# Performance work log

Measured on AMD Instinct MI355X. Metric: run time of the kernel, lower is better.

## Reference

```python
import jax, jax.numpy as jnp
import numpy as np

B, T, D = 32, 4096, 64
K = 512
COMMITMENT_COST = 0.25


def setup_inputs() -> dict:
    key = jax.random.key(0)
    kz, kw = jax.random.split(key)
    z = jax.random.normal(kz, (B, T, D), dtype=jnp.float32)
    # matches nn.init.uniform_(weight, -1/K, 1/K)
    W = jax.random.uniform(kw, (K, D), dtype=jnp.float32, minval=-1.0 / K, maxval=1.0 / K)
    return {"z": z, "W": W}


def reference(z, W):
    b, t, d = z.shape
    z_flat = z.reshape(-1, d)                                   # [N, D]
    # squared euclidean distances via ||z||^2 + ||w||^2 - 2 z.w
    dist = (jnp.sum(z_flat * z_flat, axis=1, keepdims=True)
            + jnp.sum(W * W, axis=1)
            - 2.0 * z_flat @ W.T)                               # [N, K]
    indices = jnp.argmin(dist, axis=1)                          # [N]
    z_q = W[indices].reshape(b, t, d)                           # gather
    # straight-through estimator
    z_q_st = z + jax.lax.stop_gradient(z_q - z)
    loss = COMMITMENT_COST * jnp.mean((z - jax.lax.stop_gradient(z_q_st)) ** 2)
    return z_q_st, indices.reshape(b, t), loss
```

## Files before the change

### kernel.cpp

```cpp
#include <hip/hip_runtime.h>
#include <hip/hip_bf16.h>
#include <math.h>

#define NROWS 131072
#define KC    512
#define DD    64
#define NELEM (NROWS * DD)

#define OUT_IDX_OFF  NELEM
#define OUT_LOSS_OFF (NELEM + NROWS)

#define MARGIN 3e-5f

#define WSO_CNT   0
#define WSO_LOSS  8
#define WSO_WNORM 64
#define WSO_BH    4096
#define WSO_BL    (WSO_BH + 65536)
#define WSO_LIST  (WSO_BL + 65536)

typedef __attribute__((ext_vector_type(8))) short short8;
typedef __attribute__((ext_vector_type(4))) float f32x4;

__device__ __forceinline__ short f2bf_bits(float f) {
  __hip_bfloat16 h = __float2bfloat16(f);
  short s; __builtin_memcpy(&s, &h, 2); return s;
}
__device__ __forceinline__ float bfbits2f(short s) {
  __hip_bfloat16 h; __builtin_memcpy(&h, &s, 2);
  return __bfloat162float(h);
}
__device__ __forceinline__ void cvt8(const float* __restrict__ p, short8& hi, short8& lo) {
#pragma unroll
  for (int j = 0; j < 8; j++) {
    float f = p[j];
    short hb = f2bf_bits(f);
    float r = f - bfbits2f(hb);
    hi[j] = hb;
    lo[j] = f2bf_bits(r);
  }
}

__device__ __forceinline__ float np_sumsq64(const float* __restrict__ p) {
#pragma clang fp contract(off)
  float r0 = p[0] * p[0], r1 = p[1] * p[1], r2 = p[2] * p[2], r3 = p[3] * p[3];
  float r4 = p[4] * p[4], r5 = p[5] * p[5], r6 = p[6] * p[6], r7 = p[7] * p[7];
  for (int i = 8; i < 64; i += 8) {
    r0 = r0 + p[i + 0] * p[i + 0];
    r1 = r1 + p[i + 1] * p[i + 1];
    r2 = r2 + p[i + 2] * p[i + 2];
    r3 = r3 + p[i + 3] * p[i + 3];
    r4 = r4 + p[i + 4] * p[i + 4];
    r5 = r5 + p[i + 5] * p[i + 5];
    r6 = r6 + p[i + 6] * p[i + 6];
    r7 = r7 + p[i + 7] * p[i + 7];
  }
  return ((r0 + r1) + (r2 + r3)) + ((r4 + r5) + (r6 + r7));
}

__global__ void k_prep(const float* __restrict__ W, short8* __restrict__ Bh,
                       short8* __restrict__ Bl, float* __restrict__ wnorm) {
  int gtid = blockIdx.x * blockDim.x + threadIdx.x;
  int t = gtid >> 7, rem = gtid & 127;
  int h = rem >> 6, L = rem & 63;
  int cw = (t << 4) + (L & 15);
  int dbase = (h << 5) + ((L >> 4) << 3);
  short8 hi, lo;
  cvt8(W + (cw << 6) + dbase, hi, lo);
  Bh[gtid] = hi;
  Bl[gtid] = lo;
  if (gtid < KC) wnorm[gtid] = np_sumsq64(W + (gtid << 6));
}

__global__ __launch_bounds__(256) void k_screen(
    const float* __restrict__ z, const float* __restrict__ W,
    const short8* __restrict__ Bh, const short8* __restrict__ Bl,
    const float* __restrict__ wnorm, float* __restrict__ out,
    int* __restrict__ flagList, int* __restrict__ flagCnt,
    float* __restrict__ lossSum) {
  const int lane = threadIdx.x & 63;
  const int wave = threadIdx.x >> 6;
  const int rowBase = blockIdx.x * 256 + wave * 64;
  const int m = lane & 15, quad = lane >> 4;

  short8 Ah[4][2], Al[4][2];
#pragma unroll
  for (int mt = 0; mt < 4; mt++) {
    const float* zp = z + (size_t)(rowBase + (mt << 4) + m) * DD + (quad << 3);
#pragma unroll
    for (int h = 0; h < 2; h++) cvt8(zp + (h << 5), Ah[mt][h], Al[mt][h]);
  }

  float b1[4][4], b2[4][4];
  int bi[4][4];
#pragma unroll
  for (int mt = 0; mt < 4; mt++)
#pragma unroll
    for (int r = 0; r < 4; r++) { b1[mt][r] = 1e30f; b2[mt][r] = 1e30f; bi[mt][r] = 0; }

  for (int t = 0; t < 32; t++) {
    short8 Bhf[2], Blf[2];
#pragma unroll
    for (int h = 0; h < 2; h++) {
      Bhf[h] = Bh[((t * 2 + h) << 6) + lane];
      Blf[h] = Bl[((t * 2 + h) << 6) + lane];
    }
    float wn = wnorm[(t << 4) + m];

    f32x4 acc[4] = {{0.f, 0.f, 0.f, 0.f}, {0.f, 0.f, 0.f, 0.f},
                    {0.f, 0.f, 0.f, 0.f}, {0.f, 0.f, 0.f, 0.f}};
#pragma unroll
    for (int h = 0; h < 2; h++) {
#pragma unroll
      for (int mt = 0; mt < 4; mt++)
        acc[mt] = __builtin_amdgcn_mfma_f32_16x16x32_bf16(Ah[mt][h], Bhf[h], acc[mt], 0, 0, 0);
#pragma unroll
      for (int mt = 0; mt < 4; mt++)
        acc[mt] = __builtin_amdgcn_mfma_f32_16x16x32_bf16(Al[mt][h], Bhf[h], acc[mt], 0, 0, 0);
#pragma unroll
      for (int mt = 0; mt < 4; mt++)
        acc[mt] = __builtin_amdgcn_mfma_f32_16x16x32_bf16(Ah[mt][h], Blf[h], acc[mt], 0, 0, 0);
    }

    int colv = (t << 4) + m;
#pragma unroll
    for (int mt = 0; mt < 4; mt++)
#pragma unroll
      for (int r = 0; r < 4; r++) {
        float s = fmaf(-2.0f, acc[mt][r], wn);
        if (s < b1[mt][r]) { b2[mt][r] = b1[mt][r]; b1[mt][r] = s; bi[mt][r] = colv; }
        else b2[mt][r] = fminf(b2[mt][r], s);
      }
  }

#pragma unroll
  for (int off = 1; off < 16; off <<= 1) {
#pragma unroll
    for (int mt = 0; mt < 4; mt++)
#pragma unroll
      for (int r = 0; r < 4; r++) {
        float o1 = __shfl_xor(b1[mt][r], off, 64);
        float o2 = __shfl_xor(b2[mt][r], off, 64);
        int oi = __shfl_xor(bi[mt][r], off, 64);
        if (o1 < b1[mt][r] || (o1 == b1[mt][r] && oi < bi[mt][r])) {
          b2[mt][r] = fminf(b1[mt][r], o2);
          b1[mt][r] = o1; bi[mt][r] = oi;
        } else {
          b2[mt][r] = fminf(b2[mt][r], o1);
        }
      }
  }

  float lossAcc = 0.f;
#pragma unroll
  for (int mt = 0; mt < 4; mt++)
#pragma unroll
    for (int lr = 0; lr < 16; lr++) {
      const int q = lr >> 2, r = lr & 3;
      int ki = __shfl(bi[mt][r], q << 4, 64);
      float b1r = __shfl(b1[mt][r], q << 4, 64);
      float b2r = __shfl(b2[mt][r], q << 4, 64);
      int row = rowBase + (mt << 4) + lr;
      float zv = z[(size_t)row * DD + lane];
      float w = W[(ki << 6) + lane];
      float tt = w - zv;
      float o = zv + tt;
      out[(size_t)row * DD + lane] = o;
      float dl = zv - o;
      lossAcc = fmaf(dl, dl, lossAcc);
      if (lane == 0) {
        out[OUT_IDX_OFF + row] = (float)ki;
        if (b2r - b1r < MARGIN) {
          int slot = atomicAdd(flagCnt, 1);
          flagList[slot] = row;
        }
      }
    }

#pragma unroll
  for (int off = 1; off < 64; off <<= 1) lossAcc += __shfl_xor(lossAcc, off, 64);
  if (lane == 0) atomicAdd(lossSum, lossAcc);
}

__global__ void k_refine(const float* __restrict__ z, const float* __restrict__ W,
                         const float* __restrict__ wnp, float* __restrict__ out,
                         const int* __restrict__ flagList,
                         const int* __restrict__ flagCnt,
                         float* __restrict__ lossSum) {
  int nflag = *flagCnt;
  int lane = threadIdx.x & 63;
  int wave = (blockIdx.x * blockDim.x + threadIdx.x) >> 6;
  int nWaves = (gridDim.x * blockDim.x) >> 6;

  for (int f = wave; f < nflag; f += nWaves) {
    int row = flagList[f];
    const float* zr = z + (size_t)row * DD;
    float A = np_sumsq64(zr);

    float best = 1e30f;
    int bk = 0x7fffffff;
#pragma unroll
    for (int j = 0; j < KC / 64; j++) {
      int k = lane + (j << 6);
      const float* wk = W + (k << 6);
      double cd = 0.0;
      for (int d = 0; d < DD; d++) cd = fma((double)zr[d], (double)wk[d], cd);
      float twoC = (float)(2.0 * cd);
      float dist;
      {
#pragma clang fp contract(off)
        float t1 = A + wnp[k];
        dist = t1 - twoC;
      }
      if (dist < best || (dist == best && k < bk)) { best = dist; bk = k; }
    }
#pragma unroll
    for (int off = 1; off < 64; off <<= 1) {
      float ov = __shfl_xor(best, off, 64);
      int ok = __shfl_xor(bk, off, 64);
      if (ov < best || (ov == best && ok < bk)) { best = ov; bk = ok; }
    }

    int kold = (int)out[OUT_IDX_OFF + row];
    if (bk != kold) {
      float zv = zr[lane];
      float wN = W[(bk << 6) + lane];
      float oOld = out[(size_t)row * DD + lane];
      float tN = wN - zv;
      float oN = zv + tN;
      out[(size_t)row * DD + lane] = oN;
      float dN = zv - oN, dO = zv - oOld;
      float delta = dN * dN - dO * dO;
#pragma unroll
      for (int off = 1; off < 64; off <<= 1) delta += __shfl_xor(delta, off, 64);
      if (lane == 0) {
        atomicAdd(lossSum, delta);
        out[OUT_IDX_OFF + row] = (float)bk;
      }
    }
  }
}

__global__ void k_finalize(const float* __restrict__ lossSum, float* __restrict__ out) {
  out[OUT_LOSS_OFF] = 0.25f * (*lossSum) / (float)NELEM;
}

extern "C" void kernel_launch(void* const* d_in, const int* in_sizes, int n_in,
                              void* d_out, int out_size, void* d_ws, size_t ws_size,
                              hipStream_t stream) {
  const float* z = (const float*)d_in[0];
  const float* W = (const float*)d_in[1];
  float* out = (float*)d_out;
  char* ws = (char*)d_ws;

  int* flagCnt = (int*)(ws + WSO_CNT);
  float* lossSum = (float*)(ws + WSO_LOSS);
  float* wnorm = (float*)(ws + WSO_WNORM);
  short8* Bh = (short8*)(ws + WSO_BH);
  short8* Bl = (short8*)(ws + WSO_BL);
  int* flagList = (int*)(ws + WSO_LIST);

  hipMemsetAsync(d_ws, 0, 64, stream);

  k_prep<<<16, 256, 0, stream>>>(W, Bh, Bl, wnorm);
  k_screen<<<NROWS / 256, 256, 0, stream>>>(z, W, Bh, Bl, wnorm, out,
                                            flagList, flagCnt, lossSum);
  k_refine<<<256, 256, 0, stream>>>(z, W, wnorm, out, flagList, flagCnt, lossSum);
  k_finalize<<<1, 1, 0, stream>>>(lossSum, out);
}
```

Before: 189.2 us.

## Fuse codebook prep into screen kernel and finalize loss in refine

```diff
diff --git a/kernel.cpp b/kernel.cpp
--- a/kernel.cpp
+++ b/kernel.cpp
@@ -14,30 +14,29 @@
 
 #define WSO_CNT   0
 #define WSO_LOSS  8
+#define WSO_DONE  16
 #define WSO_WNORM 64
-#define WSO_BH    4096
-#define WSO_BL    (WSO_BH + 65536)
-#define WSO_LIST  (WSO_BL + 65536)
+#define WSO_LIST  4096
 
 typedef __attribute__((ext_vector_type(8))) short short8;
 typedef __attribute__((ext_vector_type(4))) float f32x4;
 
-__device__ __forceinline__ short f2bf_bits(float f) {
+static __device__ __forceinline__ short f2bf(float f) {
   __hip_bfloat16 h = __float2bfloat16(f);
   short s; __builtin_memcpy(&s, &h, 2); return s;
 }
-__device__ __forceinline__ float bfbits2f(short s) {
-  __hip_bfloat16 h; __builtin_memcpy(&h, &s, 2);
-  return __bfloat162float(h);
-}
-__device__ __forceinline__ void cvt8(const float* __restrict__ p, short8& hi, short8& lo) {
+static __device__ __forceinline__ float bf2f(short s) {
+  unsigned u = ((unsigned)(unsigned short)s) << 16;
+  float f; __builtin_memcpy(&f, &u, 4); return f;
+}
+static __device__ __forceinline__ void split8(const float* v, short8& hi, short8& lo) {
 #pragma unroll
   for (int j = 0; j < 8; j++) {
-    float f = p[j];
-    short hb = f2bf_bits(f);
-    float r = f - bfbits2f(hb);
+    float f = v[j];
+    short hb = f2bf(f);
+    float r = f - bf2f(hb);
     hi[j] = hb;
-    lo[j] = f2bf_bits(r);
+    lo[j] = f2bf(r);
   }
 }
 
@@ -58,76 +57,84 @@
   return ((r0 + r1) + (r2 + r3)) + ((r4 + r5) + (r6 + r7));
 }
 
-__global__ void k_prep(const float* __restrict__ W, short8* __restrict__ Bh,
-                       short8* __restrict__ Bl, float* __restrict__ wnorm) {
-  int gtid = blockIdx.x * blockDim.x + threadIdx.x;
-  int t = gtid >> 7, rem = gtid & 127;
-  int h = rem >> 6, L = rem & 63;
-  int cw = (t << 4) + (L & 15);
-  int dbase = (h << 5) + ((L >> 4) << 3);
-  short8 hi, lo;
-  cvt8(W + (cw << 6) + dbase, hi, lo);
-  Bh[gtid] = hi;
-  Bl[gtid] = lo;
-  if (gtid < KC) wnorm[gtid] = np_sumsq64(W + (gtid << 6));
-}
-
-__global__ __launch_bounds__(256) void k_screen(
+__global__ __launch_bounds__(256) void k_main(
     const float* __restrict__ z, const float* __restrict__ W,
-    const short8* __restrict__ Bh, const short8* __restrict__ Bl,
-    const float* __restrict__ wnorm, float* __restrict__ out,
+    float* __restrict__ out, float* __restrict__ wnorm,
     int* __restrict__ flagList, int* __restrict__ flagCnt,
     float* __restrict__ lossSum) {
-  const int lane = threadIdx.x & 63;
-  const int wave = threadIdx.x >> 6;
-  const int rowBase = blockIdx.x * 256 + wave * 64;
+  const int tid = threadIdx.x;
+  const int lane = tid & 63;
+  const int wv = tid >> 6;
+  const int rowBase = blockIdx.x * 128 + wv * 32;
   const int m = lane & 15, quad = lane >> 4;
 
-  short8 Ah[4][2], Al[4][2];
-#pragma unroll
-  for (int mt = 0; mt < 4; mt++) {
+  if (blockIdx.x == 0) {
+    wnorm[tid] = np_sumsq64(W + (tid << 6));
+    wnorm[tid + 256] = np_sumsq64(W + ((tid + 256) << 6));
+  }
+
+  short8 Ah[2][2], Al[2][2];
+#pragma unroll
+  for (int mt = 0; mt < 2; mt++) {
     const float* zp = z + (size_t)(rowBase + (mt << 4) + m) * DD + (quad << 3);
 #pragma unroll
-    for (int h = 0; h < 2; h++) cvt8(zp + (h << 5), Ah[mt][h], Al[mt][h]);
-  }
-
-  float b1[4][4], b2[4][4];
-  int bi[4][4];
-#pragma unroll
-  for (int mt = 0; mt < 4; mt++)
+    for (int h = 0; h < 2; h++) {
+      float4 u0 = *(const float4*)(zp + (h << 5));
+      float4 u1 = *(const float4*)(zp + (h << 5) + 4);
+      float v[8] = {u0.x, u0.y, u0.z, u0.w, u1.x, u1.y, u1.z, u1.w};
+      split8(v, Ah[mt][h], Al[mt][h]);
+    }
+  }
+
+  float b1[2][4], b2[2][4];
+  int bi[2][4];
+#pragma unroll
+  for (int mt = 0; mt < 2; mt++)
 #pragma unroll
     for (int r = 0; r < 4; r++) { b1[mt][r] = 1e30f; b2[mt][r] = 1e30f; bi[mt][r] = 0; }
 
+  const float* wbase = W + (size_t)(m << 6) + (quad << 3);
   for (int t = 0; t < 32; t++) {
-    short8 Bhf[2], Blf[2];
+    const float* wp = wbase + (size_t)t * (16 * DD);
+    float4 a0 = *(const float4*)(wp);
+    float4 a1 = *(const float4*)(wp + 4);
+    float4 c0 = *(const float4*)(wp + 32);
+    float4 c1 = *(const float4*)(wp + 36);
+    float v0[8] = {a0.x, a0.y, a0.z, a0.w, a1.x, a1.y, a1.z, a1.w};
+    float v1[8] = {c0.x, c0.y, c0.z, c0.w, c1.x, c1.y, c1.z, c1.w};
+
+    float p = 0.f;
+#pragma unroll
+    for (int j = 0; j < 8; j++) p = fmaf(v0[j], v0[j], p);
+#pragma unroll
+    for (int j = 0; j < 8; j++) p = fmaf(v1[j], v1[j], p);
+    p += __shfl_xor(p, 16, 64);
+    p += __shfl_xor(p, 32, 64);
+
+    short8 Bh[2], Bl[2];
+    split8(v0, Bh[0], Bl[0]);
+    split8(v1, Bh[1], Bl[1]);
+
+    f32x4 acc[2] = {{0.f, 0.f, 0.f, 0.f}, {0.f, 0.f, 0.f, 0.f}};
 #pragma unroll
     for (int h = 0; h < 2; h++) {
-      Bhf[h] = Bh[((t * 2 + h) << 6) + lane];
-      Blf[h] = Bl[((t * 2 + h) << 6) + lane];
-    }
-    float wn = wnorm[(t << 4) + m];
-
-    f32x4 acc[4] = {{0.f, 0.f, 0.f, 0.f}, {0.f, 0.f, 0.f, 0.f},
-                    {0.f, 0.f, 0.f, 0.f}, {0.f, 0.f, 0.f, 0.f}};
-#pragma unroll
-    for (int h = 0; h < 2; h++) {
-#pragma unroll
-      for (int mt = 0; mt < 4; mt++)
-        acc[mt] = __builtin_amdgcn_mfma_f32_16x16x32_bf16(Ah[mt][h], Bhf[h], acc[mt], 0, 0, 0);
-#pragma unroll
-      for (int mt = 0; mt < 4; mt++)
-        acc[mt] = __builtin_amdgcn_mfma_f32_16x16x32_bf16(Al[mt][h], Bhf[h], acc[mt], 0, 0, 0);
-#pragma unroll
-      for (int mt = 0; mt < 4; mt++)
-        acc[mt] = __builtin_amdgcn_mfma_f32_16x16x32_bf16(Ah[mt][h], Blf[h], acc[mt], 0, 0, 0);
+#pragma unroll
+      for (int mt = 0; mt < 2; mt++)
+        acc[mt] = __builtin_amdgcn_mfma_f32_16x16x32_bf16(Ah[mt][h], Bh[h], acc[mt], 0, 0, 0);
+#pragma unroll
+      for (int mt = 0; mt < 2; mt++)
+        acc[mt] = __builtin_amdgcn_mfma_f32_16x16x32_bf16(Al[mt][h], Bh[h], acc[mt], 0, 0, 0);
+#pragma unroll
+      for (int mt = 0; mt < 2; mt++)
+        acc[mt] = __builtin_amdgcn_mfma_f32_16x16x32_bf16(Ah[mt][h], Bl[h], acc[mt], 0, 0, 0);
     }
 
     int colv = (t << 4) + m;
 #pragma unroll
-    for (int mt = 0; mt < 4; mt++)
+    for (int mt = 0; mt < 2; mt++)
 #pragma unroll
       for (int r = 0; r < 4; r++) {
-        float s = fmaf(-2.0f, acc[mt][r], wn);
+        float s = fmaf(-2.0f, acc[mt][r], p);
         if (s < b1[mt][r]) { b2[mt][r] = b1[mt][r]; b1[mt][r] = s; bi[mt][r] = colv; }
         else b2[mt][r] = fminf(b2[mt][r], s);
       }
@@ -136,7 +143,7 @@
 #pragma unroll
   for (int off = 1; off < 16; off <<= 1) {
 #pragma unroll
-    for (int mt = 0; mt < 4; mt++)
+    for (int mt = 0; mt < 2; mt++)
 #pragma unroll
       for (int r = 0; r < 4; r++) {
         float o1 = __shfl_xor(b1[mt][r], off, 64);
@@ -153,13 +160,13 @@
 
   float lossAcc = 0.f;
 #pragma unroll
-  for (int mt = 0; mt < 4; mt++)
+  for (int mt = 0; mt < 2; mt++)
 #pragma unroll
     for (int lr = 0; lr < 16; lr++) {
       const int q = lr >> 2, r = lr & 3;
       int ki = __shfl(bi[mt][r], q << 4, 64);
-      float b1r = __shfl(b1[mt][r], q << 4, 64);
-      float b2r = __shfl(b2[mt][r], q << 4, 64);
+      float gap = b2[mt][r] - b1[mt][r];
+      float gapr = __shfl(gap, q << 4, 64);
       int row = rowBase + (mt << 4) + lr;
       float zv = z[(size_t)row * DD + lane];
       float w = W[(ki << 6) + lane];
@@ -170,7 +177,7 @@
       lossAcc = fmaf(dl, dl, lossAcc);
       if (lane == 0) {
         out[OUT_IDX_OFF + row] = (float)ki;
-        if (b2r - b1r < MARGIN) {
+        if (gapr < MARGIN) {
           int slot = atomicAdd(flagCnt, 1);
           flagList[slot] = row;
         }
@@ -186,7 +193,7 @@
                          const float* __restrict__ wnp, float* __restrict__ out,
                          const int* __restrict__ flagList,
                          const int* __restrict__ flagCnt,
-                         float* __restrict__ lossSum) {
+                         float* __restrict__ lossSum, int* __restrict__ doneCnt) {
   int nflag = *flagCnt;
   int lane = threadIdx.x & 63;
   int wave = (blockIdx.x * blockDim.x + threadIdx.x) >> 6;
@@ -239,10 +246,17 @@
       }
     }
   }
-}
-
-__global__ void k_finalize(const float* __restrict__ lossSum, float* __restrict__ out) {
-  out[OUT_LOSS_OFF] = 0.25f * (*lossSum) / (float)NELEM;
+
+  __syncthreads();
+  if (threadIdx.x == 0) {
+    __threadfence();
+    int old = atomicAdd(doneCnt, 1);
+    if (old == (int)gridDim.x - 1) {
+      __threadfence();
+      float ls = atomicAdd(lossSum, 0.0f);
+      out[OUT_LOSS_OFF] = 0.25f * ls / (float)NELEM;
+    }
+  }
 }
 
 extern "C" void kernel_launch(void* const* d_in, const int* in_sizes, int n_in,
@@ -255,16 +269,12 @@
 
   int* flagCnt = (int*)(ws + WSO_CNT);
   float* lossSum = (float*)(ws + WSO_LOSS);
+  int* doneCnt = (int*)(ws + WSO_DONE);
   float* wnorm = (float*)(ws + WSO_WNORM);
-  short8* Bh = (short8*)(ws + WSO_BH);
-  short8* Bl = (short8*)(ws + WSO_BL);
   int* flagList = (int*)(ws + WSO_LIST);
 
   hipMemsetAsync(d_ws, 0, 64, stream);
 
-  k_prep<<<16, 256, 0, stream>>>(W, Bh, Bl, wnorm);
-  k_screen<<<NROWS / 256, 256, 0, stream>>>(z, W, Bh, Bl, wnorm, out,
-                                            flagList, flagCnt, lossSum);
-  k_refine<<<256, 256, 0, stream>>>(z, W, wnorm, out, flagList, flagCnt, lossSum);
-  k_finalize<<<1, 1, 0, stream>>>(lossSum, out);
-}
+  k_main<<<NROWS / 128, 256, 0, stream>>>(z, W, out, wnorm, flagList, flagCnt, lossSum);
+  k_refine<<<256, 256, 0, stream>>>(z, W, wnorm, out, flagList, flagCnt, lossSum, doneCnt);
+}
```

Measured after the change: 235.4 us. 1.24x slower.

## Fuse refine and finalize into screening kernel with inline fp64 recheck

Applied to the files above, without the earlier changes.

```diff
diff --git a/kernel.cpp b/kernel.cpp
--- a/kernel.cpp
+++ b/kernel.cpp
@@ -12,32 +12,32 @@
 
 #define MARGIN 3e-5f
 
-#define WSO_CNT   0
 #define WSO_LOSS  8
+#define WSO_DONE  16
 #define WSO_WNORM 64
 #define WSO_BH    4096
 #define WSO_BL    (WSO_BH + 65536)
-#define WSO_LIST  (WSO_BL + 65536)
 
 typedef __attribute__((ext_vector_type(8))) short short8;
 typedef __attribute__((ext_vector_type(4))) float f32x4;
 
-__device__ __forceinline__ short f2bf_bits(float f) {
+static __device__ __forceinline__ short f2bf(float f) {
   __hip_bfloat16 h = __float2bfloat16(f);
   short s; __builtin_memcpy(&s, &h, 2); return s;
 }
-__device__ __forceinline__ float bfbits2f(short s) {
-  __hip_bfloat16 h; __builtin_memcpy(&h, &s, 2);
-  return __bfloat162float(h);
-}
-__device__ __forceinline__ void cvt8(const float* __restrict__ p, short8& hi, short8& lo) {
+static __device__ __forceinline__ float bf2f(short s) {
+  unsigned u = ((unsigned)(unsigned short)s) << 16;
+  float f; __builtin_memcpy(&f, &u, 4); return f;
+}
+static __device__ __forceinline__ void cvt8(const float* __restrict__ p,
+                                            short8& hi, short8& lo) {
 #pragma unroll
   for (int j = 0; j < 8; j++) {
     float f = p[j];
-    short hb = f2bf_bits(f);
-    float r = f - bfbits2f(hb);
+    short hb = f2bf(f);
+    float r = f - bf2f(hb);
     hi[j] = hb;
-    lo[j] = f2bf_bits(r);
+    lo[j] = f2bf(r);
   }
 }
 
@@ -65,22 +65,22 @@
   int h = rem >> 6, L = rem & 63;
   int cw = (t << 4) + (L & 15);
   int dbase = (h << 5) + ((L >> 4) << 3);
+  const float* p = W + (cw << 6) + dbase;
   short8 hi, lo;
-  cvt8(W + (cw << 6) + dbase, hi, lo);
+  cvt8(p, hi, lo);
   Bh[gtid] = hi;
   Bl[gtid] = lo;
   if (gtid < KC) wnorm[gtid] = np_sumsq64(W + (gtid << 6));
 }
 
-__global__ __launch_bounds__(256) void k_screen(
+__global__ __launch_bounds__(256) void k_main(
     const float* __restrict__ z, const float* __restrict__ W,
     const short8* __restrict__ Bh, const short8* __restrict__ Bl,
     const float* __restrict__ wnorm, float* __restrict__ out,
-    int* __restrict__ flagList, int* __restrict__ flagCnt,
-    float* __restrict__ lossSum) {
+    float* __restrict__ lossSum, int* __restrict__ doneCnt) {
   const int lane = threadIdx.x & 63;
-  const int wave = threadIdx.x >> 6;
-  const int rowBase = blockIdx.x * 256 + wave * 64;
+  const int wv = threadIdx.x >> 6;
+  const int rowBase = blockIdx.x * 256 + wv * 64;
   const int m = lane & 15, quad = lane >> 4;
 
   short8 Ah[4][2], Al[4][2];
@@ -154,13 +154,42 @@
   float lossAcc = 0.f;
 #pragma unroll
   for (int mt = 0; mt < 4; mt++)
-#pragma unroll
     for (int lr = 0; lr < 16; lr++) {
       const int q = lr >> 2, r = lr & 3;
       int ki = __shfl(bi[mt][r], q << 4, 64);
       float b1r = __shfl(b1[mt][r], q << 4, 64);
       float b2r = __shfl(b2[mt][r], q << 4, 64);
       int row = rowBase + (mt << 4) + lr;
+
+      if (b2r - b1r < MARGIN) {
+        const float* zr = z + (size_t)row * DD;
+        float A = np_sumsq64(zr);
+        float best = 1e30f;
+        int bk = 0x7fffffff;
+#pragma unroll
+        for (int j = 0; j < KC / 64; j++) {
+          int k = lane + (j << 6);
+          const float* wk = W + (k << 6);
+          double cd = 0.0;
+          for (int d = 0; d < DD; d++) cd = fma((double)zr[d], (double)wk[d], cd);
+          float twoC = (float)(2.0 * cd);
+          float dist;
+          {
+#pragma clang fp contract(off)
+            float t1 = A + wnorm[k];
+            dist = t1 - twoC;
+          }
+          if (dist < best || (dist == best && k < bk)) { best = dist; bk = k; }
+        }
+#pragma unroll
+        for (int off = 1; off < 64; off <<= 1) {
+          float ov = __shfl_xor(best, off, 64);
+          int ok = __shfl_xor(bk, off, 64);
+          if (ov < best || (ov == best && ok < bk)) { best = ov; bk = ok; }
+        }
+        ki = bk;
+      }
+
       float zv = z[(size_t)row * DD + lane];
       float w = W[(ki << 6) + lane];
       float tt = w - zv;
@@ -168,81 +197,23 @@
       out[(size_t)row * DD + lane] = o;
       float dl = zv - o;
       lossAcc = fmaf(dl, dl, lossAcc);
-      if (lane == 0) {
-        out[OUT_IDX_OFF + row] = (float)ki;
-        if (b2r - b1r < MARGIN) {
-          int slot = atomicAdd(flagCnt, 1);
-          flagList[slot] = row;
-        }
-      }
+      if (lane == 0) out[OUT_IDX_OFF + row] = (float)ki;
     }
 
 #pragma unroll
   for (int off = 1; off < 64; off <<= 1) lossAcc += __shfl_xor(lossAcc, off, 64);
   if (lane == 0) atomicAdd(lossSum, lossAcc);
-}
-
-__global__ void k_refine(const float* __restrict__ z, const float* __restrict__ W,
-                         const float* __restrict__ wnp, float* __restrict__ out,
-                         const int* __restrict__ flagList,
-                         const int* __restrict__ flagCnt,
-                         float* __restrict__ lossSum) {
-  int nflag = *flagCnt;
-  int lane = threadIdx.x & 63;
-  int wave = (blockIdx.x * blockDim.x + threadIdx.x) >> 6;
-  int nWaves = (gridDim.x * blockDim.x) >> 6;
-
-  for (int f = wave; f < nflag; f += nWaves) {
-    int row = flagList[f];
-    const float* zr = z + (size_t)row * DD;
-    float A = np_sumsq64(zr);
-
-    float best = 1e30f;
-    int bk = 0x7fffffff;
-#pragma unroll
-    for (int j = 0; j < KC / 64; j++) {
-      int k = lane + (j << 6);
-      const float* wk = W + (k << 6);
-      double cd = 0.0;
-      for (int d = 0; d < DD; d++) cd = fma((double)zr[d], (double)wk[d], cd);
-      float twoC = (float)(2.0 * cd);
-      float dist;
-      {
-#pragma clang fp contract(off)
-        float t1 = A + wnp[k];
-        dist = t1 - twoC;
-      }
-      if (dist < best || (dist == best && k < bk)) { best = dist; bk = k; }
-    }
-#pragma unroll
-    for (int off = 1; off < 64; off <<= 1) {
-      float ov = __shfl_xor(best, off, 64);
-      int ok = __shfl_xor(bk, off, 64);
-      if (ov < best || (ov == best && ok < bk)) { best = ov; bk = ok; }
-    }
-
-    int kold = (int)out[OUT_IDX_OFF + row];
-    if (bk != kold) {
-      float zv = zr[lane];
-      float wN = W[(bk << 6) + lane];
-      float oOld = out[(size_t)row * DD + lane];
-      float tN = wN - zv;
-      float oN = zv + tN;
-      out[(size_t)row * DD + lane] = oN;
-      float dN = zv - oN, dO = zv - oOld;
-      float delta = dN * dN - dO * dO;
-#pragma unroll
-      for (int off = 1; off < 64; off <<= 1) delta += __shfl_xor(delta, off, 64);
-      if (lane == 0) {
-        atomicAdd(lossSum, delta);
-        out[OUT_IDX_OFF + row] = (float)bk;
-      }
-    }
-  }
-}
-
-__global__ void k_finalize(const float* __restrict__ lossSum, float* __restrict__ out) {
-  out[OUT_LOSS_OFF] = 0.25f * (*lossSum) / (float)NELEM;
+
+  __syncthreads();
+  if (threadIdx.x == 0) {
+    __threadfence();
+    int old = atomicAdd(doneCnt, 1);
+    if (old == (int)gridDim.x - 1) {
+      __threadfence();
+      float ls = atomicAdd(lossSum, 0.0f);
+      out[OUT_LOSS_OFF] = 0.25f * ls / (float)NELEM;
+    }
+  }
 }
 
 extern "C" void kernel_launch(void* const* d_in, const int* in_sizes, int n_in,
@@ -253,18 +224,15 @@
   float* out = (float*)d_out;
   char* ws = (char*)d_ws;
 
-  int* flagCnt = (int*)(ws + WSO_CNT);
   float* lossSum = (float*)(ws + WSO_LOSS);
+  int* doneCnt = (int*)(ws + WSO_DONE);
   float* wnorm = (float*)(ws + WSO_WNORM);
   short8* Bh = (short8*)(ws + WSO_BH);
   short8* Bl = (short8*)(ws + WSO_BL);
-  int* flagList = (int*)(ws + WSO_LIST);
 
   hipMemsetAsync(d_ws, 0, 64, stream);
 
   k_prep<<<16, 256, 0, stream>>>(W, Bh, Bl, wnorm);
-  k_screen<<<NROWS / 256, 256, 0, stream>>>(z, W, Bh, Bl, wnorm, out,
-                                            flagList, flagCnt, lossSum);
-  k_refine<<<256, 256, 0, stream>>>(z, W, wnorm, out, flagList, flagCnt, lossSum);
-  k_finalize<<<1, 1, 0, stream>>>(lossSum, out);
-}
+  k_main<<<NROWS / 256, 256, 0, stream>>>(z, W, Bh, Bl, wnorm, out,
+                                          lossSum, doneCnt);
+}
```

New measurement: 280.7 us. 48.3% more time.
